# Performance work log

Hardware: AMD Instinct MI355X
Metric: run time of the kernel (lower is better)

The kernel has to match this reference:

```python
import jax, jax.numpy as jnp
import numpy as np

TAU = 0.8
V_TH = 0.5
W_D1_GPI = -0.8
W_D2_STN = 0.5
W_STN_GPI = 0.6
GPI_TONIC = 0.4
NOISE = 0.1
T, B = 512, 256
N_D1, N_D2, N_GPI, N_STN = 128, 128, 64, 64


def setup_inputs() -> dict:
    key = jax.random.key(0)
    ks = jax.random.split(key, 7)
    return {
        "x": jax.random.normal(ks[0], (T, B, 2), dtype=jnp.float32),
        "dopa": jax.random.uniform(ks[1], (T, B), dtype=jnp.float32),
        "rpe": jax.random.normal(ks[2], (T, B), dtype=jnp.float32),
        "W_d1": jax.random.normal(ks[3], (N_D1, 2), dtype=jnp.float32) * 0.5,
        "W_d2": jax.random.normal(ks[4], (N_D2, 2), dtype=jnp.float32) * 0.5,
        "noise_d1": jax.random.normal(ks[5], (T, B, N_D1), dtype=jnp.float32),
        "noise_d2": jax.random.normal(ks[6], (T, B, N_D2), dtype=jnp.float32),
    }


def reference(x, dopa, rpe, W_d1, W_d2, noise_d1, noise_d2):
    """Runs T LIF steps of the spiking basal-ganglia circuit for B circuits.

    Returns gates [T, B] = d1_rate - gpi_rate per step. rpe is unused (as in source).
    """
    dt = x.dtype
    v0 = (
        jnp.zeros((B, N_D1), dt),
        jnp.zeros((B, N_D2), dt),
        jnp.zeros((B, N_GPI), dt),
        jnp.zeros((B, N_STN), dt),
    )

    def lif(v, I):
        v = TAU * v + (1.0 - TAU) * I
        s = (v >= V_TH).astype(dt)
        return v * (1.0 - s), s

    def step(carry, inp):
        v_d1, v_d2, v_gpi, v_stn = carry
        xt, dop, nd1, nd2 = inp  # [B,2], [B], [B,N], [B,N]
        d1_mod = (1.0 + dop * 0.5)[:, None]
        d2_mod = (1.0 - dop * 0.3)[:, None]
        I_d1 = jnp.einsum("bi,ni->bn", xt, W_d1) * d1_mod
        v_d1, s_d1 = lif(v_d1, I_d1 + nd1 * NOISE)
        I_d2 = jnp.einsum("bi,ni->bn", xt, W_d2) * d2_mod
        v_d2, s_d2 = lif(v_d2, I_d2 + nd2 * NOISE)
        I_stn = (s_d2.mean(axis=1) * W_D2_STN)[:, None]  # [B,1] broadcast to [B,N_STN]
        v_stn, s_stn = lif(v_stn, I_stn)
        I_gpi = (GPI_TONIC + s_d1.mean(axis=1) * W_D1_GPI + s_stn.mean(axis=1) * W_STN_GPI)[:, None]
        v_gpi, s_gpi = lif(v_gpi, I_gpi)
        gate = s_d1.mean(axis=1) - s_gpi.mean(axis=1)  # [B]
        return (v_d1, v_d2, v_gpi, v_stn), gate

    _, gates = jax.lax.scan(step, v0, (x, dopa, noise_d1, noise_d2))
    return gates  # [T, B]
```

## Files before the change

### kernel.cpp

```cpp
#include <hip/hip_runtime.h>


__global__ __launch_bounds__(320, 1) void bg_kernel(
    const float* __restrict__ x,
    const float* __restrict__ dopa,
    const float* __restrict__ Wd1,
    const float* __restrict__ Wd2,
    const float* __restrict__ nd1,
    const float* __restrict__ nd2,
    float* __restrict__ out)
{
#pragma clang fp contract(off)
    constexpr int T = 512, B = 256;
    constexpr int S = 32;
    constexpr int NCH = T / S;
    constexpr size_t TSTRIDE = (size_t)B * 128;

    __shared__ float lds_I[3][S][64][4];
    __shared__ float lds_x[T][2];
    __shared__ float lds_d[T];

    const int b    = blockIdx.x;
    const int tid  = threadIdx.x;
    const int wv   = tid >> 6;
    const int lane = tid & 63;

    for (int t = tid; t < T; t += 320) {
        const float2 xv = *(const float2*)(x + (size_t)t * (B * 2) + b * 2);
        lds_x[t][0] = xv.x;
        lds_x[t][1] = xv.y;
        lds_d[t]    = dopa[(size_t)t * B + b];
    }
    __syncthreads();

    if (wv == 0) {
        __syncthreads();

        float v1a = 0.0f, v1b = 0.0f;
        float v2a = 0.0f, v2b = 0.0f;
        float v_stn = 0.0f, v_gpi = 0.0f;
        float gate_reg = 0.0f;

        for (int i = 0; i < NCH; ++i) {
            const float (*buf)[64][4] = lds_I[i % 3];

#pragma unroll
            for (int s = 0; s < S; ++s) {
                const float4 I = *(const float4*)&buf[s][lane][0];

                v1a = 0.8f * v1a + 0.2f * I.x;
                v1b = 0.8f * v1b + 0.2f * I.y;
                v2a = 0.8f * v2a + 0.2f * I.z;
                v2b = 0.8f * v2b + 0.2f * I.w;

                const bool s1a = v1a >= 0.5f, s1b = v1b >= 0.5f;
                const bool s2a = v2a >= 0.5f, s2b = v2b >= 0.5f;
                v1a = s1a ? 0.0f : v1a;
                v1b = s1b ? 0.0f : v1b;
                v2a = s2a ? 0.0f : v2a;
                v2b = s2b ? 0.0f : v2b;

                const int c1 = __popcll(__ballot(s1a)) + __popcll(__ballot(s1b));
                const int c2 = __popcll(__ballot(s2a)) + __popcll(__ballot(s2b));
                const float mean1 = (float)c1 * 0.0078125f;
                const float mean2 = (float)c2 * 0.0078125f;

                const float I_stn = mean2 * 0.5f;
                v_stn = 0.8f * v_stn + 0.2f * I_stn;
                const float s_stn = (v_stn >= 0.5f) ? 1.0f : 0.0f;
                v_stn = (v_stn >= 0.5f) ? 0.0f : v_stn;

                const float I_gpi = (0.4f + mean1 * -0.8f) + s_stn * 0.6f;
                v_gpi = 0.8f * v_gpi + 0.2f * I_gpi;
                const float s_gpi = (v_gpi >= 0.5f) ? 1.0f : 0.0f;
                v_gpi = (v_gpi >= 0.5f) ? 0.0f : v_gpi;

                const float gate = mean1 - s_gpi;

                const int latch = ((i & 1) << 5) | s;
                gate_reg = (lane == latch) ? gate : gate_reg;
            }

            if (i & 1) {
                const int t0 = (i - 1) * S;
                out[(size_t)(t0 + lane) * B + b] = gate_reg;
            }

            __syncthreads();
        }
    } else {
        const float4 w1 = *(const float4*)(Wd1 + 4 * lane);
        const float4 w2 = *(const float4*)(Wd2 + 4 * lane);
        const float* n1b = nd1 + (size_t)b * 128 + 2 * lane;
        const float* n2b = nd2 + (size_t)b * 128 + 2 * lane;
        const int p0 = wv - 1;

        auto stage = [&](int c, int bf) {
            const int tbase = c * S;
            float2 a1[8], a2[8];
#pragma unroll
            for (int j = 0; j < 8; ++j) {
                const int t = tbase + p0 + 4 * j;
                a1[j] = *(const float2*)(n1b + (size_t)t * TSTRIDE);
                a2[j] = *(const float2*)(n2b + (size_t)t * TSTRIDE);
            }
#pragma unroll
            for (int j = 0; j < 8; ++j) {
                const int s = p0 + 4 * j;
                const int t = tbase + s;
                const float xx = lds_x[t][0], xy = lds_x[t][1];
                const float dop = lds_d[t];

                const float m1 = 1.0f + dop * 0.5f;
                const float m2 = 1.0f - dop * 0.3f;

                const float dot1a = __builtin_fmaf(xy, w1.y, xx * w1.x);
                const float dot1b = __builtin_fmaf(xy, w1.w, xx * w1.z);
                const float dot2a = __builtin_fmaf(xy, w2.y, xx * w2.x);
                const float dot2b = __builtin_fmaf(xy, w2.w, xx * w2.z);

                float4 I;
                I.x = dot1a * m1 + a1[j].x * 0.1f;
                I.y = dot1b * m1 + a1[j].y * 0.1f;
                I.z = dot2a * m2 + a2[j].x * 0.1f;
                I.w = dot2b * m2 + a2[j].y * 0.1f;

                *(float4*)&lds_I[bf][s][lane][0] = I;
            }
        };

        stage(0, 0);
        stage(1, 1);
        __syncthreads();

        for (int i = 0; i < NCH; ++i) {
            if (i + 2 < NCH) stage(i + 2, (i + 2) % 3);
            __syncthreads();
        }
    }
}

extern "C" void kernel_launch(void* const* d_in, const int* in_sizes, int n_in,
                              void* d_out, int out_size, void* d_ws, size_t ws_size,
                              hipStream_t stream) {
    const float* x    = (const float*)d_in[0];
    const float* dopa = (const float*)d_in[1];
    const float* Wd1  = (const float*)d_in[3];
    const float* Wd2  = (const float*)d_in[4];
    const float* nd1  = (const float*)d_in[5];
    const float* nd2  = (const float*)d_in[6];
    float* out = (float*)d_out;

    bg_kernel<<<dim3(256), dim3(320), 0, stream>>>(x, dopa, Wd1, Wd2, nd1, nd2, out);
}
```

Baseline: 191.8 us.

## Stream noise directly to LDS via async loads and move input math to consumer wave

Producer waves no longer compute the input currents. They issue global_load_lds DMA copies of the raw noise rows straight into a 4-deep LDS ring and pace themselves with explicit vmcnt waits and s_barrier. The consumer wave now computes the dot products, the dopamine modulation and the noise scaling inline before each LIF step. This aims to remove producer register round-trips and VALU work and to deepen prefetch, at the cost of lengthening the serial critical path in the single consumer wave.

```diff
diff --git a/kernel.cpp b/kernel.cpp
--- a/kernel.cpp
+++ b/kernel.cpp
@@ -1,5 +1,12 @@
 #include <hip/hip_runtime.h>
 
+
+typedef const __attribute__((address_space(1))) void* gptr1_t;
+typedef __attribute__((address_space(3))) void* lptr3_t;
+
+__device__ __forceinline__ void gload_lds16(const float* g, float* l) {
+    __builtin_amdgcn_global_load_lds((gptr1_t)g, (lptr3_t)l, 16, 0, 0);
+}
 
 __global__ __launch_bounds__(320, 1) void bg_kernel(
     const float* __restrict__ x,
@@ -14,9 +21,10 @@
     constexpr int T = 512, B = 256;
     constexpr int S = 32;
     constexpr int NCH = T / S;
+    constexpr int NBUF = 4;
     constexpr size_t TSTRIDE = (size_t)B * 128;
 
-    __shared__ float lds_I[3][S][64][4];
+    __shared__ float lds_raw[NBUF][S][256];
     __shared__ float lds_x[T][2];
     __shared__ float lds_d[T];
 
@@ -34,6 +42,9 @@
     __syncthreads();
 
     if (wv == 0) {
+        const float4 w1 = *(const float4*)(Wd1 + 4 * lane);
+        const float4 w2 = *(const float4*)(Wd2 + 4 * lane);
+
         __syncthreads();
 
         float v1a = 0.0f, v1b = 0.0f;
@@ -42,16 +53,31 @@
         float gate_reg = 0.0f;
 
         for (int i = 0; i < NCH; ++i) {
-            const float (*buf)[64][4] = lds_I[i % 3];
+            const float (*buf)[256] = lds_raw[i & (NBUF - 1)];
 
 #pragma unroll
             for (int s = 0; s < S; ++s) {
-                const float4 I = *(const float4*)&buf[s][lane][0];
+                const int t = i * S + s;
+                const float2 a1 = *(const float2*)&buf[s][2 * lane];
+                const float2 a2 = *(const float2*)&buf[s][128 + 2 * lane];
+                const float xx  = lds_x[t][0], xy = lds_x[t][1];
+                const float dop = lds_d[t];
 
-                v1a = 0.8f * v1a + 0.2f * I.x;
-                v1b = 0.8f * v1b + 0.2f * I.y;
-                v2a = 0.8f * v2a + 0.2f * I.z;
-                v2b = 0.8f * v2b + 0.2f * I.w;
+                const float m1 = 1.0f + dop * 0.5f;
+                const float m2 = 1.0f - dop * 0.3f;
+                const float dot1a = __builtin_fmaf(xy, w1.y, xx * w1.x);
+                const float dot1b = __builtin_fmaf(xy, w1.w, xx * w1.z);
+                const float dot2a = __builtin_fmaf(xy, w2.y, xx * w2.x);
+                const float dot2b = __builtin_fmaf(xy, w2.w, xx * w2.z);
+                const float Ix = dot1a * m1 + a1.x * 0.1f;
+                const float Iy = dot1b * m1 + a1.y * 0.1f;
+                const float Iz = dot2a * m2 + a2.x * 0.1f;
+                const float Iw = dot2b * m2 + a2.y * 0.1f;
+
+                v1a = 0.8f * v1a + 0.2f * Ix;
+                v1b = 0.8f * v1b + 0.2f * Iy;
+                v2a = 0.8f * v2a + 0.2f * Iz;
+                v2b = 0.8f * v2b + 0.2f * Iw;
 
                 const bool s1a = v1a >= 0.5f, s1b = v1b >= 0.5f;
                 const bool s2a = v2a >= 0.5f, s2b = v2b >= 0.5f;
@@ -89,53 +115,43 @@
             __syncthreads();
         }
     } else {
-        const float4 w1 = *(const float4*)(Wd1 + 4 * lane);
-        const float4 w2 = *(const float4*)(Wd2 + 4 * lane);
-        const float* n1b = nd1 + (size_t)b * 128 + 2 * lane;
-        const float* n2b = nd2 + (size_t)b * 128 + 2 * lane;
-        const int p0 = wv - 1;
+        const int p0 = (wv - 1) * 8;
+        const float* srcb = (lane < 32)
+            ? (nd1 + (size_t)b * 128 + 4 * lane)
+            : (nd2 + (size_t)b * 128 + 4 * (lane - 32));
 
-        auto stage = [&](int c, int bf) {
-            const int tbase = c * S;
-            float2 a1[8], a2[8];
+        auto stage = [&](int c) {
+            float* dst = &lds_raw[c & (NBUF - 1)][0][0];
 #pragma unroll
-            for (int j = 0; j < 8; ++j) {
-                const int t = tbase + p0 + 4 * j;
-                a1[j] = *(const float2*)(n1b + (size_t)t * TSTRIDE);
-                a2[j] = *(const float2*)(n2b + (size_t)t * TSTRIDE);
-            }
-#pragma unroll
-            for (int j = 0; j < 8; ++j) {
-                const int s = p0 + 4 * j;
-                const int t = tbase + s;
-                const float xx = lds_x[t][0], xy = lds_x[t][1];
-                const float dop = lds_d[t];
-
-                const float m1 = 1.0f + dop * 0.5f;
-                const float m2 = 1.0f - dop * 0.3f;
-
-                const float dot1a = __builtin_fmaf(xy, w1.y, xx * w1.x);
-                const float dot1b = __builtin_fmaf(xy, w1.w, xx * w1.z);
-                const float dot2a = __builtin_fmaf(xy, w2.y, xx * w2.x);
-                const float dot2b = __builtin_fmaf(xy, w2.w, xx * w2.z);
-
-                float4 I;
-                I.x = dot1a * m1 + a1[j].x * 0.1f;
-                I.y = dot1b * m1 + a1[j].y * 0.1f;
-                I.z = dot2a * m2 + a2[j].x * 0.1f;
-                I.w = dot2b * m2 + a2[j].y * 0.1f;
-
-                *(float4*)&lds_I[bf][s][lane][0] = I;
+            for (int k = 0; k < 8; ++k) {
+                const int s = p0 + k;
+                const int t = c * S + s;
+                gload_lds16(srcb + (size_t)t * TSTRIDE, dst + (size_t)s * 256);
             }
         };
 
-        stage(0, 0);
-        stage(1, 1);
-        __syncthreads();
+        stage(0);
+        stage(1);
+        stage(2);
+        __builtin_amdgcn_sched_barrier(0);
+        asm volatile("s_waitcnt vmcnt(16)" ::: "memory");
+        __builtin_amdgcn_sched_barrier(0);
+        __builtin_amdgcn_s_barrier();
+        __builtin_amdgcn_sched_barrier(0);
 
         for (int i = 0; i < NCH; ++i) {
-            if (i + 2 < NCH) stage(i + 2, (i + 2) % 3);
-            __syncthreads();
+            if (i + 3 < NCH) stage(i + 3);
+            __builtin_amdgcn_sched_barrier(0);
+            if (i <= 12) {
+                asm volatile("s_waitcnt vmcnt(16)" ::: "memory");
+            } else if (i == 13) {
+                asm volatile("s_waitcnt vmcnt(8)" ::: "memory");
+            } else if (i == 14) {
+                asm volatile("s_waitcnt vmcnt(0)" ::: "memory");
+            }
+            __builtin_amdgcn_sched_barrier(0);
+            __builtin_amdgcn_s_barrier();
+            __builtin_amdgcn_sched_barrier(0);
         }
     }
 }
```

Measured after the change: 206.0 us. 1.07x slower.
